# Kernel tuning notes

Measured on AMD Instinct MI355X. Metric: run time of the kernel, lower is better.

Reference implementation:

```python
import jax, jax.numpy as jnp
import numpy as np

B, S, DIM = 2, 2048, 1536
H = 12            # n_heads (SIGMA)
HD = DIM // H     # head_dim = 128
SIGMA = 12        # anchors per query: 6 local + 4 strided + 2 global
STRIDE_STEP = 5   # SOPFR


def setup_inputs() -> dict:
    key = jax.random.key(0)
    k0, k1, k2 = jax.random.split(key, 3)
    s = 0.02
    return {
        "x": jax.random.normal(k0, (B, S, DIM), dtype=jnp.float32),
        "Wqkv": jax.random.normal(k1, (DIM, 3 * DIM), dtype=jnp.float32) * s,
        "bqkv": jnp.zeros((3 * DIM,), dtype=jnp.float32),
        "Wout": jax.random.normal(k2, (DIM, DIM), dtype=jnp.float32) * s,
        "bout": jnp.zeros((DIM,), dtype=jnp.float32),
        # Egyptian-fraction init: [W_LOCAL, W_STRIDE, W_GLOBAL] = [1/2, 1/3, 1/6]
        "group_scale": jnp.array([0.5, 1.0 / 3.0, 1.0 / 6.0], dtype=jnp.float32),
    }


def _anchor_indices(seq_len):
    # (S, 12) int32: 6 local offsets, 4 strided offsets, then global {0, S-1}
    pos = jnp.arange(seq_len, dtype=jnp.int32)
    offs = jnp.array([-3, -2, -1, 1, 2, 3,
                      -2 * STRIDE_STEP, -STRIDE_STEP, STRIDE_STEP, 2 * STRIDE_STEP],
                     dtype=jnp.int32)
    a = jnp.clip(pos[:, None] + offs[None, :], 0, seq_len - 1)
    glob = jnp.stack([jnp.zeros_like(pos), jnp.full_like(pos, seq_len - 1)], axis=1)
    return jnp.concatenate([a, glob], axis=1)


def reference(x, Wqkv, bqkv, Wout, bout, group_scale):
    b, s, d_model = x.shape
    # QKV projection -> (3, B, H, S, HD)
    qkv = (x @ Wqkv + bqkv).reshape(b, s, 3, H, HD).transpose(2, 0, 3, 1, 4)
    q, k, v = qkv[0], qkv[1], qkv[2]
    scale = HD ** -0.5

    anchor = _anchor_indices(s)                 # (S, SIGMA)
    k_anchors = jnp.take(k, anchor, axis=2)     # (B, H, S, SIGMA, HD)
    v_anchors = jnp.take(v, anchor, axis=2)     # (B, H, S, SIGMA, HD)

    attn = jnp.einsum('bhsd,bhsad->bhsa', q, k_anchors) * scale

    gw = jax.nn.softmax(group_scale)            # (3,)
    weight_per_anchor = jnp.concatenate([
        jnp.broadcast_to(gw[0], (6,)),   # local
        jnp.broadcast_to(gw[1], (4,)),   # strided
        jnp.broadcast_to(gw[2], (2,)),   # global
    ])                                          # (SIGMA,)
    attn = attn + jnp.log(weight_per_anchor)    # broadcast over (B,H,S,·)

    attn = jax.nn.softmax(attn, axis=-1)
    attn = jnp.nan_to_num(attn, nan=0.0)

    out = jnp.einsum('bhsa,bhsad->bhsd', attn, v_anchors)
    out = out.transpose(0, 2, 1, 3).reshape(b, s, d_model)
    return out @ Wout + bout
```

## Files before the change

kernel.cpp:

```cpp
#include <hip/hip_runtime.h>
#include <hip/hip_bf16.h>
#include <cstdint>
#include <math.h>

#define B_    2
#define S_    2048
#define DIM_  1536
#define H_    12
#define HD_   128
#define TRI_  4608
#define M_    4096

typedef __attribute__((ext_vector_type(8))) __bf16 bf16x8;
typedef __attribute__((ext_vector_type(4))) __bf16 bf16x4;
typedef __attribute__((ext_vector_type(4))) float  floatx4;

typedef __attribute__((address_space(3))) uint8_t       lds_u8;
typedef const __attribute__((address_space(1))) uint8_t glob_u8;

__global__ __launch_bounds__(256) void cvt_f32_bf16(const float* __restrict__ in,
                                                    __bf16* __restrict__ out, int n4) {
    int i = blockIdx.x * blockDim.x + threadIdx.x;
    if (i >= n4) return;
    float4 v = ((const float4*)in)[i];
    bf16x4 o;
    o.x = (__bf16)v.x; o.y = (__bf16)v.y; o.z = (__bf16)v.z; o.w = (__bf16)v.w;
    *(bf16x4*)(out + (size_t)i * 4) = o;
}

__global__ __launch_bounds__(256) void transpose2(const float* __restrict__ W1,
                                                  __bf16* __restrict__ O1,
                                                  const float* __restrict__ W2,
                                                  __bf16* __restrict__ O2) {
    const int T1 = (TRI_ / 64) * (DIM_ / 64);
    int blk = blockIdx.x;
    const float* in; __bf16* out; int R, C, c0, r0;
    if (blk < T1) {
        in = W1; out = O1; R = DIM_; C = TRI_;
        c0 = (blk % (TRI_ / 64)) * 64; r0 = (blk / (TRI_ / 64)) * 64;
    } else {
        blk -= T1;
        in = W2; out = O2; R = DIM_; C = DIM_;
        c0 = (blk % (DIM_ / 64)) * 64; r0 = (blk / (DIM_ / 64)) * 64;
    }
    __shared__ float tile[64][65];
    const int t = threadIdx.x;
    const int c4 = t & 15, r = t >> 4;
    #pragma unroll
    for (int i = 0; i < 64; i += 16) {
        float4 v = *(const float4*)&in[(size_t)(r0 + r + i) * C + c0 + c4 * 4];
        tile[r + i][c4 * 4 + 0] = v.x;
        tile[r + i][c4 * 4 + 1] = v.y;
        tile[r + i][c4 * 4 + 2] = v.z;
        tile[r + i][c4 * 4 + 3] = v.w;
    }
    __syncthreads();
    const int cc = t >> 2, ch = t & 3;
    #pragma unroll
    for (int cho = 0; cho < 8; cho += 4) {
        int chh = ch + cho;
        bf16x8 o;
        #pragma unroll
        for (int k = 0; k < 8; ++k) o[k] = (__bf16)tile[chh * 8 + k][cc];
        *(bf16x8*)&out[(size_t)(c0 + cc) * R + r0 + chh * 8] = o;
    }
}

__global__ __launch_bounds__(256, 3) void gemm_qkv(const __bf16* __restrict__ A,
                                                   const __bf16* __restrict__ Bt,
                                                   const float*  __restrict__ bias,
                                                   __bf16* __restrict__ Cout,
                                                   int Mdim, int Ndim, int Kdim) {
    __shared__ __align__(16) __bf16 sA[128 * 64];
    __shared__ __align__(16) __bf16 sB[192 * 64];

    const int ntiles = Ndim / 192;
    const int tile_n = blockIdx.x % ntiles;
    const int tile_m = blockIdx.x / ntiles;
    const int m0 = tile_m << 7, n0 = tile_n * 192;

    const int tid  = threadIdx.x;
    const int lane = tid & 63;
    const int wave = tid >> 6;
    const int wm = (wave >> 1) * 64;
    const int wn = (wave & 1) * 96;

    floatx4 acc[4][6] = {};

    const int lr8 = lane >> 3;
    const int swz = (((lane & 7) ^ lr8) * 8);
    const int row  = lane & 15;
    const int quad = lane >> 4;
    const int xr   = row & 7;

    for (int k0 = 0; k0 < Kdim; k0 += 64) {
        #pragma unroll
        for (int c = 0; c < 4; ++c) {
            int r0 = wave * 32 + c * 8;
            const __bf16* ga = A + (size_t)(m0 + r0 + lr8) * Kdim + k0 + swz;
            __builtin_amdgcn_global_load_lds((glob_u8*)ga, (lds_u8*)&sA[r0 * 64], 16, 0, 0);
        }
        #pragma unroll
        for (int c = 0; c < 6; ++c) {
            int r0 = wave * 48 + c * 8;
            const __bf16* gb = Bt + (size_t)(n0 + r0 + lr8) * Kdim + k0 + swz;
            __builtin_amdgcn_global_load_lds((glob_u8*)gb, (lds_u8*)&sB[r0 * 64], 16, 0, 0);
        }
        __syncthreads();

        #pragma unroll
        for (int ks = 0; ks < 2; ++ks) {
            const int ko = ((ks * 4 + quad) ^ xr) * 8;
            bf16x8 af[4], bfr[6];
            #pragma unroll
            for (int i = 0; i < 4; ++i)
                af[i] = *(const bf16x8*)&sA[(wm + i * 16 + row) * 64 + ko];
            #pragma unroll
            for (int j = 0; j < 6; ++j)
                bfr[j] = *(const bf16x8*)&sB[(wn + j * 16 + row) * 64 + ko];
            #pragma unroll
            for (int i = 0; i < 4; ++i)
                #pragma unroll
                for (int j = 0; j < 6; ++j)
                    acc[i][j] = __builtin_amdgcn_mfma_f32_16x16x32_bf16(af[i], bfr[j], acc[i][j], 0, 0, 0);
        }
        __syncthreads();
    }

    #pragma unroll
    for (int j = 0; j < 6; ++j) {
        int gc = n0 + wn + j * 16 + row;
        float bv = bias[gc];
        #pragma unroll
        for (int i = 0; i < 4; ++i) {
            #pragma unroll
            for (int r = 0; r < 4; ++r) {
                int gr = m0 + wm + i * 16 + quad * 4 + r;
                Cout[(size_t)gr * Ndim + gc] = (__bf16)(acc[i][j][r] + bv);
            }
        }
    }
}

__global__ __launch_bounds__(128) void gemm_out(const __bf16* __restrict__ A,
                                                const __bf16* __restrict__ Bt,
                                                const float*  __restrict__ bias,
                                                float* __restrict__ Cout,
                                                int Mdim, int Ndim, int Kdim) {
    __shared__ __align__(16) __bf16 sA[64 * 64];
    __shared__ __align__(16) __bf16 sB[128 * 64];

    const int ntiles = Ndim >> 7;
    const int tile_n = blockIdx.x % ntiles;
    const int tile_m = blockIdx.x / ntiles;
    const int m0 = tile_m << 6, n0 = tile_n << 7;

    const int tid  = threadIdx.x;
    const int lane = tid & 63;
    const int wave = tid >> 6;
    const int wn = wave * 64;

    floatx4 acc[4][4] = {};

    const int lr8 = lane >> 3;
    const int swz = (((lane & 7) ^ lr8) * 8);
    const int row  = lane & 15;
    const int quad = lane >> 4;
    const int xr   = row & 7;

    for (int k0 = 0; k0 < Kdim; k0 += 64) {
        #pragma unroll
        for (int c = 0; c < 4; ++c) {
            int r0 = wave * 32 + c * 8;
            const __bf16* ga = A + (size_t)(m0 + r0 + lr8) * Kdim + k0 + swz;
            __builtin_amdgcn_global_load_lds((glob_u8*)ga, (lds_u8*)&sA[r0 * 64], 16, 0, 0);
        }
        #pragma unroll
        for (int c = 0; c < 8; ++c) {
            int r0 = wave * 64 + c * 8;
            const __bf16* gb = Bt + (size_t)(n0 + r0 + lr8) * Kdim + k0 + swz;
            __builtin_amdgcn_global_load_lds((glob_u8*)gb, (lds_u8*)&sB[r0 * 64], 16, 0, 0);
        }
        __syncthreads();

        #pragma unroll
        for (int ks = 0; ks < 2; ++ks) {
            const int ko = ((ks * 4 + quad) ^ xr) * 8;
            bf16x8 af[4], bfr[4];
            #pragma unroll
            for (int i = 0; i < 4; ++i) {
                af[i]  = *(const bf16x8*)&sA[(i * 16 + row) * 64 + ko];
                bfr[i] = *(const bf16x8*)&sB[(wn + i * 16 + row) * 64 + ko];
            }
            #pragma unroll
            for (int i = 0; i < 4; ++i)
                #pragma unroll
                for (int j = 0; j < 4; ++j)
                    acc[i][j] = __builtin_amdgcn_mfma_f32_16x16x32_bf16(af[i], bfr[j], acc[i][j], 0, 0, 0);
        }
        __syncthreads();
    }

    #pragma unroll
    for (int j = 0; j < 4; ++j) {
        int gc = n0 + wn + j * 16 + row;
        float bv = bias[gc];
        #pragma unroll
        for (int i = 0; i < 4; ++i) {
            #pragma unroll
            for (int r = 0; r < 4; ++r) {
                int gr = m0 + i * 16 + quad * 4 + r;
                Cout[(size_t)gr * Ndim + gc] = acc[i][j][r] + bv;
            }
        }
    }
}

__global__ __launch_bounds__(192) void anchor_attn(const __bf16* __restrict__ qkv,
                                                   const float* __restrict__ group_scale,
                                                   __bf16* __restrict__ attn_out) {
    const int bs = blockIdx.x;
    const int b  = bs >> 11;
    const int s  = bs & 2047;
    const int t  = threadIdx.x;
    const int h  = t >> 4;
    const int tt = t & 15;
    const int d0 = tt * 8;

    float g0 = group_scale[0], g1 = group_scale[1], g2 = group_scale[2];
    float gm = fmaxf(g0, fmaxf(g1, g2));
    float e0 = __expf(g0 - gm), e1 = __expf(g1 - gm), e2 = __expf(g2 - gm);
    float ls = __logf(e0 + e1 + e2);
    float lw0 = g0 - gm - ls, lw1 = g1 - gm - ls, lw2 = g2 - gm - ls;

    const size_t rowbase = (size_t)(b * S_ + s) * TRI_ + h * HD_ + d0;
    bf16x8 qv = *(const bf16x8*)(qkv + rowbase);
    float q[8];
    #pragma unroll
    for (int k = 0; k < 8; ++k) q[k] = (float)qv[k];

    int idxs[12];
    const int offs[10] = {-3, -2, -1, 1, 2, 3, -10, -5, 5, 10};
    #pragma unroll
    for (int a = 0; a < 10; ++a) {
        int tgt = s + offs[a];
        idxs[a] = min(max(tgt, 0), S_ - 1);
    }
    idxs[10] = 0; idxs[11] = S_ - 1;

    const float scale = 0.08838834764831845f;
    float p[12];
    float mx = -1e30f;
    #pragma unroll
    for (int a = 0; a < 12; ++a) {
        const __bf16* kp = qkv + (size_t)(b * S_ + idxs[a]) * TRI_ + DIM_ + h * HD_ + d0;
        bf16x8 kv = *(const bf16x8*)kp;
        float d = 0.f;
        #pragma unroll
        for (int k = 0; k < 8; ++k) d += q[k] * (float)kv[k];
        d += __shfl_xor(d, 1); d += __shfl_xor(d, 2);
        d += __shfl_xor(d, 4); d += __shfl_xor(d, 8);
        float sc = d * scale + (a < 6 ? lw0 : (a < 10 ? lw1 : lw2));
        p[a] = sc;
        mx = fmaxf(mx, sc);
    }
    float l = 0.f;
    #pragma unroll
    for (int a = 0; a < 12; ++a) { p[a] = __expf(p[a] - mx); l += p[a]; }
    float inv = 1.0f / l;

    float o[8] = {};
    #pragma unroll
    for (int a = 0; a < 12; ++a) {
        const __bf16* vp = qkv + (size_t)(b * S_ + idxs[a]) * TRI_ + 2 * DIM_ + h * HD_ + d0;
        bf16x8 vv = *(const bf16x8*)vp;
        #pragma unroll
        for (int k = 0; k < 8; ++k) o[k] += p[a] * (float)vv[k];
    }
    bf16x8 ov;
    #pragma unroll
    for (int k = 0; k < 8; ++k) ov[k] = (__bf16)(o[k] * inv);
    *(bf16x8*)(attn_out + (size_t)(b * S_ + s) * DIM_ + h * HD_ + d0) = ov;
}

extern "C" void kernel_launch(void* const* d_in, const int* in_sizes, int n_in,
                              void* d_out, int out_size, void* d_ws, size_t ws_size,
                              hipStream_t stream) {
    const float* x    = (const float*)d_in[0];
    const float* Wqkv = (const float*)d_in[1];
    const float* bqkv = (const float*)d_in[2];
    const float* Wout = (const float*)d_in[3];
    const float* bout = (const float*)d_in[4];
    const float* gsc  = (const float*)d_in[5];
    float* out = (float*)d_out;

    char* ws = (char*)d_ws;
    __bf16* x_bf   = (__bf16*)(ws);
    __bf16* WqkvT  = (__bf16*)(ws + 12582912);
    __bf16* WoutT  = (__bf16*)(ws + 12582912 + 14155776);
    __bf16* qkv    = (__bf16*)(ws + 12582912 + 14155776 + 4718592);
    __bf16* attn   = (__bf16*)(ws + 12582912 + 14155776 + 4718592 + 37748736);

    {
        int n4 = (M_ * DIM_) / 4;
        cvt_f32_bf16<<<(n4 + 255) / 256, 256, 0, stream>>>(x, x_bf, n4);
    }
    {
        int nblk = (TRI_ / 64) * (DIM_ / 64) + (DIM_ / 64) * (DIM_ / 64);
        transpose2<<<nblk, 256, 0, stream>>>(Wqkv, WqkvT, Wout, WoutT);
    }

    gemm_qkv<<<(M_ / 128) * (TRI_ / 192), 256, 0, stream>>>(
        x_bf, WqkvT, bqkv, qkv, M_, TRI_, DIM_);

    anchor_attn<<<B_ * S_, 192, 0, stream>>>(qkv, gsc, attn);

    gemm_out<<<(M_ / 64) * (DIM_ / 128), 128, 0, stream>>>(
        attn, WoutT, bout, out, M_, DIM_, DIM_);
}
```

Before: 240.6 us.

## Split-K output GEMM with atomics, larger tiles, fuse prep kernels with zeroing

Merges the x conversion and weight transpose kernels into one prep launch that also zeroes the output buffer. The output GEMM moves to 128x128 tiles with 4 waves and splits K into two halves, so the grid keeps a similar number of blocks while each tile is larger. Partial results are combined with float atomicAdd, and only the first half adds the bias. In exchange, the zeroing pass costs extra writes and the atomics add traffic and make the summation order nondeterministic.

After: 252.7 us. 5.0% more time.

```diff
diff --git a/kernel.cpp b/kernel.cpp
--- a/kernel.cpp
+++ b/kernel.cpp
@@ -18,22 +18,35 @@
 typedef __attribute__((address_space(3))) uint8_t       lds_u8;
 typedef const __attribute__((address_space(1))) uint8_t glob_u8;
 
-__global__ __launch_bounds__(256) void cvt_f32_bf16(const float* __restrict__ in,
-                                                    __bf16* __restrict__ out, int n4) {
-    int i = blockIdx.x * blockDim.x + threadIdx.x;
-    if (i >= n4) return;
-    float4 v = ((const float4*)in)[i];
-    bf16x4 o;
-    o.x = (__bf16)v.x; o.y = (__bf16)v.y; o.z = (__bf16)v.z; o.w = (__bf16)v.w;
-    *(bf16x4*)(out + (size_t)i * 4) = o;
-}
-
-__global__ __launch_bounds__(256) void transpose2(const float* __restrict__ W1,
-                                                  __bf16* __restrict__ O1,
-                                                  const float* __restrict__ W2,
-                                                  __bf16* __restrict__ O2) {
+__global__ __launch_bounds__(256) void prep(const float* __restrict__ W1,
+                                            __bf16* __restrict__ O1,
+                                            const float* __restrict__ W2,
+                                            __bf16* __restrict__ O2,
+                                            const float* __restrict__ x,
+                                            __bf16* __restrict__ x_bf,
+                                            float* __restrict__ outz) {
     const int T1 = (TRI_ / 64) * (DIM_ / 64);
+    const int T2 = (DIM_ / 64) * (DIM_ / 64);
+    const int NC = (M_ * DIM_) / 1024;
     int blk = blockIdx.x;
+    const int t = threadIdx.x;
+
+    if (blk >= T1 + T2) {
+        blk -= T1 + T2;
+        if (blk < NC) {
+            int i = blk * 256 + t;
+            float4 v = ((const float4*)x)[i];
+            bf16x4 o;
+            o.x = (__bf16)v.x; o.y = (__bf16)v.y; o.z = (__bf16)v.z; o.w = (__bf16)v.w;
+            *(bf16x4*)(x_bf + (size_t)i * 4) = o;
+        } else {
+            blk -= NC;
+            int i = blk * 256 + t;
+            ((float4*)outz)[i] = make_float4(0.f, 0.f, 0.f, 0.f);
+        }
+        return;
+    }
+
     const float* in; __bf16* out; int R, C, c0, r0;
     if (blk < T1) {
         in = W1; out = O1; R = DIM_; C = TRI_;
@@ -44,7 +57,6 @@
         c0 = (blk % (DIM_ / 64)) * 64; r0 = (blk / (DIM_ / 64)) * 64;
     }
     __shared__ float tile[64][65];
-    const int t = threadIdx.x;
     const int c4 = t & 15, r = t >> 4;
     #pragma unroll
     for (int i = 0; i < 64; i += 16) {
@@ -142,23 +154,30 @@
     }
 }
 
-__global__ __launch_bounds__(128) void gemm_out(const __bf16* __restrict__ A,
-                                                const __bf16* __restrict__ Bt,
-                                                const float*  __restrict__ bias,
-                                                float* __restrict__ Cout,
-                                                int Mdim, int Ndim, int Kdim) {
-    __shared__ __align__(16) __bf16 sA[64 * 64];
+__global__ __launch_bounds__(256, 3) void gemm_out(const __bf16* __restrict__ A,
+                                                   const __bf16* __restrict__ Bt,
+                                                   const float*  __restrict__ bias,
+                                                   float* __restrict__ Cout,
+                                                   int Mdim, int Ndim, int Kdim) {
+    __shared__ __align__(16) __bf16 sA[128 * 64];
     __shared__ __align__(16) __bf16 sB[128 * 64];
 
     const int ntiles = Ndim >> 7;
-    const int tile_n = blockIdx.x % ntiles;
-    const int tile_m = blockIdx.x / ntiles;
-    const int m0 = tile_m << 6, n0 = tile_n << 7;
+    const int half = (Mdim >> 7) * ntiles;
+    int idx = blockIdx.x;
+    const int slice = idx >= half;
+    if (slice) idx -= half;
+    const int tile_n = idx % ntiles;
+    const int tile_m = idx / ntiles;
+    const int m0 = tile_m << 7, n0 = tile_n << 7;
+    const int kbeg = slice ? (Kdim >> 1) : 0;
+    const int kend = kbeg + (Kdim >> 1);
 
     const int tid  = threadIdx.x;
     const int lane = tid & 63;
     const int wave = tid >> 6;
-    const int wn = wave * 64;
+    const int wm = (wave >> 1) * 64;
+    const int wn = (wave & 1) * 64;
 
     floatx4 acc[4][4] = {};
 
@@ -168,16 +187,12 @@
     const int quad = lane >> 4;
     const int xr   = row & 7;
 
-    for (int k0 = 0; k0 < Kdim; k0 += 64) {
+    for (int k0 = kbeg; k0 < kend; k0 += 64) {
         #pragma unroll
         for (int c = 0; c < 4; ++c) {
             int r0 = wave * 32 + c * 8;
             const __bf16* ga = A + (size_t)(m0 + r0 + lr8) * Kdim + k0 + swz;
             __builtin_amdgcn_global_load_lds((glob_u8*)ga, (lds_u8*)&sA[r0 * 64], 16, 0, 0);
-        }
-        #pragma unroll
-        for (int c = 0; c < 8; ++c) {
-            int r0 = wave * 64 + c * 8;
             const __bf16* gb = Bt + (size_t)(n0 + r0 + lr8) * Kdim + k0 + swz;
             __builtin_amdgcn_global_load_lds((glob_u8*)gb, (lds_u8*)&sB[r0 * 64], 16, 0, 0);
         }
@@ -189,7 +204,7 @@
             bf16x8 af[4], bfr[4];
             #pragma unroll
             for (int i = 0; i < 4; ++i) {
-                af[i]  = *(const bf16x8*)&sA[(i * 16 + row) * 64 + ko];
+                af[i]  = *(const bf16x8*)&sA[(wm + i * 16 + row) * 64 + ko];
                 bfr[i] = *(const bf16x8*)&sB[(wn + i * 16 + row) * 64 + ko];
             }
             #pragma unroll
@@ -204,13 +219,13 @@
     #pragma unroll
     for (int j = 0; j < 4; ++j) {
         int gc = n0 + wn + j * 16 + row;
-        float bv = bias[gc];
+        float bv = slice ? 0.f : bias[gc];
         #pragma unroll
         for (int i = 0; i < 4; ++i) {
             #pragma unroll
             for (int r = 0; r < 4; ++r) {
-                int gr = m0 + i * 16 + quad * 4 + r;
-                Cout[(size_t)gr * Ndim + gc] = acc[i][j][r] + bv;
+                int gr = m0 + wm + i * 16 + quad * 4 + r;
+                atomicAdd(&Cout[(size_t)gr * Ndim + gc], acc[i][j][r] + bv);
             }
         }
     }
@@ -302,12 +317,9 @@
     __bf16* attn   = (__bf16*)(ws + 12582912 + 14155776 + 4718592 + 37748736);
 
     {
-        int n4 = (M_ * DIM_) / 4;
-        cvt_f32_bf16<<<(n4 + 255) / 256, 256, 0, stream>>>(x, x_bf, n4);
-    }
-    {
-        int nblk = (TRI_ / 64) * (DIM_ / 64) + (DIM_ / 64) * (DIM_ / 64);
-        transpose2<<<nblk, 256, 0, stream>>>(Wqkv, WqkvT, Wout, WoutT);
+        int nblk = (TRI_ / 64) * (DIM_ / 64) + (DIM_ / 64) * (DIM_ / 64)
+                 + (M_ * DIM_) / 1024 + (M_ * DIM_) / 1024;
+        prep<<<nblk, 256, 0, stream>>>(Wqkv, WqkvT, Wout, WoutT, x, x_bf, out);
     }
 
     gemm_qkv<<<(M_ / 128) * (TRI_ / 192), 256, 0, stream>>>(
@@ -315,6 +327,6 @@
 
     anchor_attn<<<B_ * S_, 192, 0, stream>>>(qkv, gsc, attn);
 
-    gemm_out<<<(M_ / 64) * (DIM_ / 128), 128, 0, stream>>>(
+    gemm_out<<<2 * (M_ / 128) * (DIM_ / 128), 256, 0, stream>>>(
         attn, WoutT, bout, out, M_, DIM_, DIM_);
 }
```
